# Performance work log

Hardware: AMD Instinct MI355X
Metric: run time of the kernel (lower is better)

The kernel has to match this reference:

```python
import jax, jax.numpy as jnp
import numpy as np
import math

B, L, DM = 8, 4096, 512            # batch, seq len (LQ == LK required by mean-fill quirk), model dim
DK, DV, C = 512, 512, 5            # projected dims, sampling factor
U_K = min(int(C * math.ceil(math.log(L))), L)  # 45 sampled keys
U_Q = min(int(C * math.ceil(math.log(L))), L)  # 45 top queries
SCALE = 1.0 / math.sqrt(DM)        # original divides by sqrt(d) where d = input dm


def setup_inputs() -> dict:
    key = jax.random.key(0)
    ks = jax.random.split(key, 10)
    w = 1.0 / math.sqrt(DM)
    # sample key indices per batch WITHOUT replacement (matches jax.random.choice(replace=False))
    kidx = jax.vmap(lambda k: jax.random.choice(k, L, shape=(U_K,), replace=False))(
        jax.random.split(ks[9], B)).astype(jnp.int32)
    return {
        "Q": jax.random.normal(ks[0], (B, L, DM), jnp.float32),
        "K": jax.random.normal(ks[1], (B, L, DM), jnp.float32),
        "V": jax.random.normal(ks[2], (B, L, DM), jnp.float32),
        "WQ": jax.random.normal(ks[3], (DM, DK), jnp.float32) * w,
        "bQ": jnp.zeros((DK,), jnp.float32),
        "WK": jax.random.normal(ks[4], (DM, DK), jnp.float32) * w,
        "bK": jnp.zeros((DK,), jnp.float32),
        "WV": jax.random.normal(ks[5], (DM, DV), jnp.float32) * w,
        "bV": jnp.zeros((DV,), jnp.float32),
        "kidx": kidx,
    }


def reference(Q, K, V, WQ, bQ, WK, bK, WV, bV, kidx):
    # dense projections (compute-dominant)
    Qp = Q @ WQ + bQ          # [B, L, DK]
    Kp = K @ WK + bK          # [B, L, DK]
    Vp = V @ WV + bV          # [B, L, DV]

    def per_sample(qp, kp, vp, idx):
        kbar = kp[idx]                                 # [U_K, DK] random key gather
        sbar = qp @ kbar.T                             # [L, U_K] sampled scores
        meas = jnp.max(sbar, axis=1) - jnp.mean(sbar, axis=1)  # sparsity measurement [L]
        _, I = jax.lax.top_k(meas, U_Q)                # top-u query indices
        qbar = qp[I]                                   # [U_Q, DK]
        attn = jax.nn.softmax(qbar @ kp.T * SCALE, axis=-1)    # [U_Q, L]
        s1 = attn @ vp                                 # [U_Q, DV]
        # faithful quirk: mean over FEATURE axis of V, broadcast to [L, DV]
        base = jnp.broadcast_to(jnp.mean(vp, axis=1, keepdims=True), (L, DV))
        return base.at[I].set(s1)                      # scatter selected rows

    return jax.vmap(per_sample)(Qp, Kp, Vp, kidx)      # [B, L, DV]
```

## Files before the change

kernel.cpp:

```cpp
#include <hip/hip_runtime.h>
#include <math.h>

static constexpr int B_ = 8;
static constexpr int L_ = 4096;
static constexpr int D_ = 512;
static constexpr int U_ = 45;
static constexpr float SCALE_ = 0.04419417382415922f;

static constexpr size_t OFF_WVMEAN = 0;
static constexpr size_t OFF_BV     = 512;
static constexpr size_t OFF_WQT    = 576;
static constexpr size_t OFF_WKT    = OFF_WQT + 262144;
static constexpr size_t OFF_KBAR   = OFF_WKT + 262144;
static constexpr size_t OFF_KW     = OFF_KBAR + 184320;
static constexpr size_t OFF_CVEC   = OFF_KW + 184320;
static constexpr size_t OFF_MEAS   = OFF_CVEC + 384;
static constexpr size_t OFF_TOPI   = OFF_MEAS + 32768;
static constexpr size_t OFF_QBAR   = OFF_TOPI + 384;
static constexpr size_t OFF_QW     = OFF_QBAR + 184320;
static constexpr size_t OFF_DVEC   = OFF_QW + 184320;
static constexpr size_t OFF_SC     = OFF_DVEC + 384;
static constexpr size_t OFF_PART   = OFF_SC + 1474560;
static constexpr size_t OFF_SMMX   = OFF_PART + 1474560;
static constexpr size_t OFF_SMIV   = OFF_SMMX + 512;
static constexpr size_t OFF_S1     = OFF_SMIV + 512;

__device__ __forceinline__ float wave_sum(float v) {
  #pragma unroll
  for (int m = 32; m; m >>= 1) v += __shfl_xor(v, m, 64);
  return v;
}
__device__ __forceinline__ float wave_max(float v) {
  #pragma unroll
  for (int m = 32; m; m >>= 1) v = fmaxf(v, __shfl_xor(v, m, 64));
  return v;
}

__global__ __launch_bounds__(256) void prep_k(const float* __restrict__ WQ,
    const float* __restrict__ WK, float* __restrict__ wqt, float* __restrict__ wkt,
    const float* __restrict__ WV, const float* __restrict__ bV,
    float* __restrict__ wvmean, float* __restrict__ bvout) {
  const int z = blockIdx.z;
  const int t = threadIdx.x + threadIdx.y * 32;
  if (z < 2) {
    const float* src = z ? WK : WQ;
    float* dst = z ? wkt : wqt;
    __shared__ float tile[32][33];
    int tx = threadIdx.x, ty = threadIdx.y;
    int x = blockIdx.x * 32 + tx;
    int y0 = blockIdx.y * 32;
    for (int r = ty; r < 32; r += 8) tile[r][tx] = src[(size_t)(y0 + r) * 512 + x];
    __syncthreads();
    int xo = y0 + tx;
    int yo0 = blockIdx.x * 32;
    for (int r = ty; r < 32; r += 8) dst[(size_t)(yo0 + r) * 512 + xo] = tile[tx][r];
    return;
  }
  if (blockIdx.y != 0 || blockIdx.x >= 8) return;
  int w = t >> 6, lane = t & 63;
  const float4* W4 = (const float4*)WV;
  int mbase = (blockIdx.x * 4 + w) * 16;
  for (int i = 0; i < 16; ++i) {
    int m = mbase + i;
    float4 a = W4[(size_t)m * 128 + lane];
    float4 c = W4[(size_t)m * 128 + 64 + lane];
    float s = ((a.x + a.y) + (a.z + a.w)) + ((c.x + c.y) + (c.z + c.w));
    s = wave_sum(s);
    if (lane == 0) wvmean[m] = s * (1.0f / 512.0f);
  }
  if (blockIdx.x == 0 && w == 0) {
    const float4* b4 = (const float4*)bV;
    float4 a = b4[lane], c = b4[64 + lane];
    float s = ((a.x + a.y) + (a.z + a.w)) + ((c.x + c.y) + (c.z + c.w));
    s = wave_sum(s);
    if (lane == 0) bvout[0] = s * (1.0f / 512.0f);
  }
}

__global__ __launch_bounds__(512) void projpair_k(const float* __restrict__ src,
    const int* __restrict__ idx, const float* __restrict__ W1, const float* __restrict__ b1,
    const float* __restrict__ avec, float* __restrict__ aux,
    const float* __restrict__ W2T, float* __restrict__ outp) {
  const int blk = blockIdx.x;
  const int b = blk / U_, j = blk % U_;
  const int t = threadIdx.x;
  __shared__ float rowA[512];
  __shared__ float rowB[512];
  __shared__ float red[8];

  const float* srow = idx ? (src + ((size_t)b * L_ + idx[b * U_ + j]) * 512)
                          : (src + ((size_t)(b * U_ + j)) * 512);
  rowA[t] = srow[t];
  __syncthreads();

  float a = b1[t];
  #pragma unroll 8
  for (int m = 0; m < 512; ++m) a = fmaf(rowA[m], W1[(size_t)m * 512 + t], a);

  if (aux) {
    float v = wave_sum(a * avec[t]);
    if ((t & 63) == 0) red[t >> 6] = v;
  }
  rowB[t] = a;
  __syncthreads();
  if (aux && t == 0) {
    float s2 = 0.f;
    #pragma unroll
    for (int k = 0; k < 8; ++k) s2 += red[k];
    aux[b * U_ + j] = s2;
  }

  float o = 0.f;
  #pragma unroll 8
  for (int m = 0; m < 512; ++m) o = fmaf(rowB[m], W2T[(size_t)m * 512 + t], o);
  outp[((size_t)(b * U_ + j)) * 512 + t] = o;
}

__global__ __launch_bounds__(512) void s1red_k(const float* __restrict__ part,
    const float* __restrict__ WV, const float* __restrict__ bV, float* __restrict__ s1) {
  const int blk = blockIdx.x;
  const int t = threadIdx.x;
  __shared__ float rowA[512];
  const size_t base = (size_t)blk * 512 + t;
  float s = 0.f;
  #pragma unroll
  for (int ls = 0; ls < 8; ++ls) s += part[(size_t)ls * 184320 + base];
  rowA[t] = s;
  __syncthreads();
  float o = bV[t];
  #pragma unroll 8
  for (int m = 0; m < 512; ++m) o = fmaf(rowA[m], WV[(size_t)m * 512 + t], o);
  s1[(size_t)blk * 512 + t] = o;
}

__global__ __launch_bounds__(256) void meas2_k(const float* __restrict__ Q,
    const float* __restrict__ kw, const float* __restrict__ cvec, float* __restrict__ meas) {
  const int b = blockIdx.y;
  const int l0 = blockIdx.x * 64;
  const int t = threadIdx.x;
  const int tx = t & 15, ty = t >> 4;
  const int rswz = (ty >> 1) & 3;

  __shared__ float Qs[64][68];
  __shared__ float Ks[48][68];

  float acc[4][3];
  #pragma unroll
  for (int i = 0; i < 4; ++i) { acc[i][0] = 0.f; acc[i][1] = 0.f; acc[i][2] = 0.f; }

  const float4* Q4  = (const float4*)(Q + ((size_t)b * L_ + l0) * 512);
  const float4* kw4 = (const float4*)(kw + (size_t)b * U_ * 512);

  float4 pq[4], pk[3];
  int lr[4], lc[4], kr[3], kc[3];
  #pragma unroll
  for (int p = 0; p < 4; ++p) { int idx = p * 256 + t; lr[p] = idx >> 4; lc[p] = idx & 15; }
  #pragma unroll
  for (int p = 0; p < 3; ++p) { int idx = p * 256 + t; kr[p] = idx >> 4; kc[p] = idx & 15; }

  #pragma unroll
  for (int p = 0; p < 4; ++p) pq[p] = Q4[(size_t)lr[p] * 128 + lc[p]];
  #pragma unroll
  for (int p = 0; p < 3; ++p)
    pk[p] = (kr[p] < U_) ? kw4[(size_t)kr[p] * 128 + kc[p]] : make_float4(0.f, 0.f, 0.f, 0.f);

  #pragma unroll
  for (int p = 0; p < 4; ++p) {
    int sw = (lr[p] >> 3) & 3;
    *(float4*)&Qs[lr[p]][(lc[p] ^ sw) * 4] = pq[p];
  }
  #pragma unroll
  for (int p = 0; p < 3; ++p) *(float4*)&Ks[kr[p]][kc[p] * 4] = pk[p];
  __syncthreads();

  for (int it = 0; it < 8; ++it) {
    if (it < 7) {
      int k0 = (it + 1) * 16;
      #pragma unroll
      for (int p = 0; p < 4; ++p) pq[p] = Q4[(size_t)lr[p] * 128 + k0 + lc[p]];
      #pragma unroll
      for (int p = 0; p < 3; ++p)
        pk[p] = (kr[p] < U_) ? kw4[(size_t)kr[p] * 128 + k0 + kc[p]] : make_float4(0.f, 0.f, 0.f, 0.f);
    }
    #pragma unroll 4
    for (int kk4 = 0; kk4 < 16; ++kk4) {
      float4 kv0 = *(const float4*)&Ks[tx * 3 + 0][kk4 * 4];
      float4 kv1 = *(const float4*)&Ks[tx * 3 + 1][kk4 * 4];
      float4 kv2 = *(const float4*)&Ks[tx * 3 + 2][kk4 * 4];
      int qc = (kk4 ^ rswz) * 4;
      #pragma unroll
      for (int i = 0; i < 4; ++i) {
        float4 qv = *(const float4*)&Qs[ty * 4 + i][qc];
        acc[i][0] = fmaf(qv.x, kv0.x, acc[i][0]); acc[i][0] = fmaf(qv.y, kv0.y, acc[i][0]);
        acc[i][0] = fmaf(qv.z, kv0.z, acc[i][0]); acc[i][0] = fmaf(qv.w, kv0.w, acc[i][0]);
        acc[i][1] = fmaf(qv.x, kv1.x, acc[i][1]); acc[i][1] = fmaf(qv.y, kv1.y, acc[i][1]);
        acc[i][1] = fmaf(qv.z, kv1.z, acc[i][1]); acc[i][1] = fmaf(qv.w, kv1.w, acc[i][1]);
        acc[i][2] = fmaf(qv.x, kv2.x, acc[i][2]); acc[i][2] = fmaf(qv.y, kv2.y, acc[i][2]);
        acc[i][2] = fmaf(qv.z, kv2.z, acc[i][2]); acc[i][2] = fmaf(qv.w, kv2.w, acc[i][2]);
      }
    }
    __syncthreads();
    if (it < 7) {
      #pragma unroll
      for (int p = 0; p < 4; ++p) {
        int sw = (lr[p] >> 3) & 3;
        *(float4*)&Qs[lr[p]][(lc[p] ^ sw) * 4] = pq[p];
      }
      #pragma unroll
      for (int p = 0; p < 3; ++p) *(float4*)&Ks[kr[p]][kc[p] * 4] = pk[p];
      __syncthreads();
    }
  }

  const bool valid = (tx < 15);
  float c0 = 0.f, c1 = 0.f, c2 = 0.f;
  if (valid) {
    c0 = cvec[b * U_ + tx * 3 + 0];
    c1 = cvec[b * U_ + tx * 3 + 1];
    c2 = cvec[b * U_ + tx * 3 + 2];
  }
  #pragma unroll
  for (int i = 0; i < 4; ++i) {
    float s0 = acc[i][0] + c0, s1 = acc[i][1] + c1, s2 = acc[i][2] + c2;
    float jmax = valid ? fmaxf(fmaxf(s0, s1), s2) : -3.4e38f;
    float jsum = valid ? (s0 + s1 + s2) : 0.f;
    #pragma unroll
    for (int m = 8; m; m >>= 1) {
      jmax = fmaxf(jmax, __shfl_xor(jmax, m, 64));
      jsum += __shfl_xor(jsum, m, 64);
    }
    if (tx == 0) meas[(size_t)b * L_ + l0 + ty * 4 + i] = jmax - jsum * (1.0f / 45.0f);
  }
}

__global__ __launch_bounds__(256) void scores2_k(const float* __restrict__ K,
    const float* __restrict__ qw, const float* __restrict__ dvec, float* __restrict__ sc) {
  const int b = blockIdx.y;
  const int l0 = blockIdx.x * 64;
  const int t = threadIdx.x;
  const int tx = t & 15, ty = t >> 4;
  const int rswz = (ty >> 1) & 3;

  __shared__ float Qs[64][68];
  __shared__ float Ks[48][68];

  float acc[4][3];
  #pragma unroll
  for (int i = 0; i < 4; ++i) { acc[i][0] = 0.f; acc[i][1] = 0.f; acc[i][2] = 0.f; }

  const float4* K4  = (const float4*)(K + ((size_t)b * L_ + l0) * 512);
  const float4* qw4 = (const float4*)(qw + (size_t)b * U_ * 512);

  float4 pq[4], pk[3];
  int lr[4], lc[4], kr[3], kc[3];
  #pragma unroll
  for (int p = 0; p < 4; ++p) { int idx = p * 256 + t; lr[p] = idx >> 4; lc[p] = idx & 15; }
  #pragma unroll
  for (int p = 0; p < 3; ++p) { int idx = p * 256 + t; kr[p] = idx >> 4; kc[p] = idx & 15; }

  #pragma unroll
  for (int p = 0; p < 4; ++p) pq[p] = K4[(size_t)lr[p] * 128 + lc[p]];
  #pragma unroll
  for (int p = 0; p < 3; ++p)
    pk[p] = (kr[p] < U_) ? qw4[(size_t)kr[p] * 128 + kc[p]] : make_float4(0.f, 0.f, 0.f, 0.f);

  #pragma unroll
  for (int p = 0; p < 4; ++p) {
    int sw = (lr[p] >> 3) & 3;
    *(float4*)&Qs[lr[p]][(lc[p] ^ sw) * 4] = pq[p];
  }
  #pragma unroll
  for (int p = 0; p < 3; ++p) *(float4*)&Ks[kr[p]][kc[p] * 4] = pk[p];
  __syncthreads();

  for (int it = 0; it < 8; ++it) {
    if (it < 7) {
      int k0 = (it + 1) * 16;
      #pragma unroll
      for (int p = 0; p < 4; ++p) pq[p] = K4[(size_t)lr[p] * 128 + k0 + lc[p]];
      #pragma unroll
      for (int p = 0; p < 3; ++p)
        pk[p] = (kr[p] < U_) ? qw4[(size_t)kr[p] * 128 + k0 + kc[p]] : make_float4(0.f, 0.f, 0.f, 0.f);
    }
    #pragma unroll 4
    for (int kk4 = 0; kk4 < 16; ++kk4) {
      float4 kv0 = *(const float4*)&Ks[tx * 3 + 0][kk4 * 4];
      float4 kv1 = *(const float4*)&Ks[tx * 3 + 1][kk4 * 4];
      float4 kv2 = *(const float4*)&Ks[tx * 3 + 2][kk4 * 4];
      int qc = (kk4 ^ rswz) * 4;
      #pragma unroll
      for (int i = 0; i < 4; ++i) {
        float4 qv = *(const float4*)&Qs[ty * 4 + i][qc];
        acc[i][0] = fmaf(qv.x, kv0.x, acc[i][0]); acc[i][0] = fmaf(qv.y, kv0.y, acc[i][0]);
        acc[i][0] = fmaf(qv.z, kv0.z, acc[i][0]); acc[i][0] = fmaf(qv.w, kv0.w, acc[i][0]);
        acc[i][1] = fmaf(qv.x, kv1.x, acc[i][1]); acc[i][1] = fmaf(qv.y, kv1.y, acc[i][1]);
        acc[i][1] = fmaf(qv.z, kv1.z, acc[i][1]); acc[i][1] = fmaf(qv.w, kv1.w, acc[i][1]);
        acc[i][2] = fmaf(qv.x, kv2.x, acc[i][2]); acc[i][2] = fmaf(qv.y, kv2.y, acc[i][2]);
        acc[i][2] = fmaf(qv.z, kv2.z, acc[i][2]); acc[i][2] = fmaf(qv.w, kv2.w, acc[i][2]);
      }
    }
    __syncthreads();
    if (it < 7) {
      #pragma unroll
      for (int p = 0; p < 4; ++p) {
        int sw = (lr[p] >> 3) & 3;
        *(float4*)&Qs[lr[p]][(lc[p] ^ sw) * 4] = pq[p];
      }
      #pragma unroll
      for (int p = 0; p < 3; ++p) *(float4*)&Ks[kr[p]][kc[p] * 4] = pk[p];
      __syncthreads();
    }
  }

  if (tx < 15) {
    float d0 = dvec[b * U_ + tx * 3 + 0];
    float d1 = dvec[b * U_ + tx * 3 + 1];
    float d2 = dvec[b * U_ + tx * 3 + 2];
    #pragma unroll
    for (int i = 0; i < 4; ++i) {
      int l = l0 + ty * 4 + i;
      sc[((size_t)(b * U_ + tx * 3 + 0)) * 4096 + l] = (acc[i][0] + d0) * SCALE_;
      sc[((size_t)(b * U_ + tx * 3 + 1)) * 4096 + l] = (acc[i][1] + d1) * SCALE_;
      sc[((size_t)(b * U_ + tx * 3 + 2)) * 4096 + l] = (acc[i][2] + d2) * SCALE_;
    }
  }
}

__global__ __launch_bounds__(256) void topk_k(const float* __restrict__ meas, int* __restrict__ topI) {
  int b = blockIdx.x, t = threadIdx.x;
  __shared__ unsigned long long keys[4096];
  __shared__ unsigned long long wred[4];
  for (int i = t; i < 4096; i += 256) {
    float m = meas[(size_t)b * 4096 + i];
    unsigned u = __float_as_uint(m);
    u = (u & 0x80000000u) ? ~u : (u | 0x80000000u);
    keys[i] = ((unsigned long long)u << 32) | (unsigned)(4095 - i);
  }
  __syncthreads();
  for (int it = 0; it < U_; ++it) {
    unsigned long long lm = 0ull;
    for (int i = t; i < 4096; i += 256) { unsigned long long k = keys[i]; lm = k > lm ? k : lm; }
    #pragma unroll
    for (int m = 32; m; m >>= 1) { unsigned long long o = __shfl_xor(lm, m, 64); lm = o > lm ? o : lm; }
    if ((t & 63) == 0) wred[t >> 6] = lm;
    __syncthreads();
    if (t == 0) {
      unsigned long long f = wred[0];
      for (int k2 = 1; k2 < 4; ++k2) f = wred[k2] > f ? wred[k2] : f;
      int idxl = 4095 - (int)(f & 0xFFFFFFFFull);
      topI[b * U_ + it] = idxl;
      keys[idxl] = 0ull;
    }
    __syncthreads();
  }
}

__global__ __launch_bounds__(256) void smred_k(const float* __restrict__ sc,
    float* __restrict__ mxb, float* __restrict__ ivb) {
  int row = blockIdx.x;
  int t = threadIdx.x;
  const float4* s4 = (const float4*)(sc + (size_t)row * 4096);
  __shared__ float red[4];
  float4 v[4];
  #pragma unroll
  for (int p = 0; p < 4; ++p) v[p] = s4[t + p * 256];
  float lmax = -3.4e38f;
  #pragma unroll
  for (int p = 0; p < 4; ++p)
    lmax = fmaxf(lmax, fmaxf(fmaxf(v[p].x, v[p].y), fmaxf(v[p].z, v[p].w)));
  lmax = wave_max(lmax);
  if ((t & 63) == 0) red[t >> 6] = lmax;
  __syncthreads();
  float mx = fmaxf(fmaxf(red[0], red[1]), fmaxf(red[2], red[3]));
  __syncthreads();
  float lsum = 0.f;
  #pragma unroll
  for (int p = 0; p < 4; ++p)
    lsum += expf(v[p].x - mx) + expf(v[p].y - mx) + expf(v[p].z - mx) + expf(v[p].w - mx);
  lsum = wave_sum(lsum);
  if ((t & 63) == 0) red[t >> 6] = lsum;
  __syncthreads();
  if (t == 0) {
    mxb[row] = mx;
    ivb[row] = 1.0f / (red[0] + red[1] + red[2] + red[3]);
  }
}

__device__ __forceinline__ float4 sm4(float4 v, float m, float iv) {
  return make_float4(expf(v.x - m) * iv, expf(v.y - m) * iv,
                     expf(v.z - m) * iv, expf(v.w - m) * iv);
}

__global__ __launch_bounds__(256) void attnv5_k(const float* __restrict__ V,
    const float* __restrict__ attn, const float* __restrict__ mxb,
    const float* __restrict__ ivb, float* __restrict__ part) {
  const int b = blockIdx.x, ks = blockIdx.y, dh = blockIdx.z;
  const int d0 = dh * 64;
  const int t = threadIdx.x;
  const int tx = t & 15, ty = t >> 4;

  __shared__ float As[2][48][68];
  __shared__ float Vs[2][64][68];

  const float* attnb = attn + (size_t)b * U_ * 4096 + (size_t)ks * 512;
  const float* Vb = V + ((size_t)b * L_ + (size_t)ks * 512) * 512 + d0;

  const int vrow = t >> 4, vc4 = t & 15;
  int arow[3], ac4[3], arr[3];
  float mxv[3], ivv[3];
  #pragma unroll
  for (int p = 0; p < 3; ++p) {
    int idx = p * 256 + t;
    arow[p] = idx >> 4; ac4[p] = idx & 15;
    arr[p] = arow[p] < U_ ? arow[p] : U_ - 1;
    mxv[p] = mxb[b * U_ + arr[p]];
    ivv[p] = ivb[b * U_ + arr[p]];
  }

  float4 pv0, pv1, pv2, pv3, pa0, pa1, pa2;

#define ISSUE(S) do { const int lb_ = (S) * 64;                                  \
    pv0 = *(const float4*)&Vb[(size_t)(lb_ + vrow +  0) * 512 + vc4 * 4];        \
    pv1 = *(const float4*)&Vb[(size_t)(lb_ + vrow + 16) * 512 + vc4 * 4];        \
    pv2 = *(const float4*)&Vb[(size_t)(lb_ + vrow + 32) * 512 + vc4 * 4];        \
    pv3 = *(const float4*)&Vb[(size_t)(lb_ + vrow + 48) * 512 + vc4 * 4];        \
    pa0 = *(const float4*)&attnb[(size_t)arr[0] * 4096 + lb_ + ac4[0] * 4];      \
    pa1 = *(const float4*)&attnb[(size_t)arr[1] * 4096 + lb_ + ac4[1] * 4];      \
    pa2 = *(const float4*)&attnb[(size_t)arr[2] * 4096 + lb_ + ac4[2] * 4];      \
  } while (0)

#define COMMIT(BUF) do {                                                         \
    *(float4*)&Vs[BUF][vrow +  0][vc4 * 4] = pv0;                                \
    *(float4*)&Vs[BUF][vrow + 16][vc4 * 4] = pv1;                                \
    *(float4*)&Vs[BUF][vrow + 32][vc4 * 4] = pv2;                                \
    *(float4*)&Vs[BUF][vrow + 48][vc4 * 4] = pv3;                                \
    *(float4*)&As[BUF][arow[0]][ac4[0] * 4] = sm4(pa0, mxv[0], ivv[0]);          \
    *(float4*)&As[BUF][arow[1]][ac4[1] * 4] = sm4(pa1, mxv[1], ivv[1]);          \
    *(float4*)&As[BUF][arow[2]][ac4[2] * 4] = sm4(pa2, mxv[2], ivv[2]);          \
  } while (0)

  float4 acc0 = make_float4(0.f, 0.f, 0.f, 0.f);
  float4 acc1 = make_float4(0.f, 0.f, 0.f, 0.f);
  float4 acc2 = make_float4(0.f, 0.f, 0.f, 0.f);

  ISSUE(0);
  asm volatile("s_waitcnt vmcnt(0)" ::: "memory");
  COMMIT(0);
  ISSUE(1);
  asm volatile("s_waitcnt lgkmcnt(0)" ::: "memory");
  __builtin_amdgcn_s_barrier();
  __builtin_amdgcn_sched_barrier(0);

  #pragma unroll 1
  for (int s = 0; s < 8; ++s) {
    const int rb = s & 1;
    #pragma unroll 4
    for (int l4 = 0; l4 < 16; ++l4) {
      float4 q0 = *(const float4*)&As[rb][tx * 3 + 0][l4 * 4];
      float4 q1 = *(const float4*)&As[rb][tx * 3 + 1][l4 * 4];
      float4 q2 = *(const float4*)&As[rb][tx * 3 + 2][l4 * 4];
      #pragma unroll
      for (int j = 0; j < 4; ++j) {
        float4 v = *(const float4*)&Vs[rb][l4 * 4 + j][ty * 4];
        float a0 = (j == 0) ? q0.x : (j == 1) ? q0.y : (j == 2) ? q0.z : q0.w;
        float a1 = (j == 0) ? q1.x : (j == 1) ? q1.y : (j == 2) ? q1.z : q1.w;
        float a2 = (j == 0) ? q2.x : (j == 1) ? q2.y : (j == 2) ? q2.z : q2.w;
        acc0.x = fmaf(a0, v.x, acc0.x); acc0.y = fmaf(a0, v.y, acc0.y);
        acc0.z = fmaf(a0, v.z, acc0.z); acc0.w = fmaf(a0, v.w, acc0.w);
        acc1.x = fmaf(a1, v.x, acc1.x); acc1.y = fmaf(a1, v.y, acc1.y);
        acc1.z = fmaf(a1, v.z, acc1.z); acc1.w = fmaf(a1, v.w, acc1.w);
        acc2.x = fmaf(a2, v.x, acc2.x); acc2.y = fmaf(a2, v.y, acc2.y);
        acc2.z = fmaf(a2, v.z, acc2.z); acc2.w = fmaf(a2, v.w, acc2.w);
      }
    }
    if (s + 1 < 8) {
      asm volatile("s_waitcnt vmcnt(0)" ::: "memory");
      COMMIT((s + 1) & 1);
      if (s + 2 < 8) ISSUE(s + 2);
      asm volatile("s_waitcnt lgkmcnt(0)" ::: "memory");
      __builtin_amdgcn_s_barrier();
      __builtin_amdgcn_sched_barrier(0);
    }
  }
#undef ISSUE
#undef COMMIT

  {
    float* dstbase = part + (((size_t)(ks * 8 + b)) * U_) * 512 + d0 + ty * 4;
    int i0 = tx * 3;
    if (i0 + 0 < U_) *(float4*)(dstbase + (size_t)(i0 + 0) * 512) = acc0;
    if (i0 + 1 < U_) *(float4*)(dstbase + (size_t)(i0 + 1) * 512) = acc1;
    if (i0 + 2 < U_) *(float4*)(dstbase + (size_t)(i0 + 2) * 512) = acc2;
  }
}

__global__ __launch_bounds__(256) void output_k(const float* __restrict__ V,
    const float* __restrict__ wvmean, const float* __restrict__ bvp,
    const int* __restrict__ topI, const float* __restrict__ s1, float* __restrict__ outp) {
  int b = blockIdx.y, tile = blockIdx.x;
  int l0 = tile * 64;
  int t = threadIdx.x, w = t >> 6, lane = t & 63;
  __shared__ int sel[64];
  if (t < 64) sel[t] = -1;
  __syncthreads();
  if (t < U_) {
    int lj = topI[b * U_ + t] - l0;
    if (lj >= 0 && lj < 64) sel[lj] = t;
  }
  __syncthreads();
  const float4* wv4 = (const float4*)wvmean;
  float4 wa = wv4[lane], wb = wv4[64 + lane];
  float bv = bvp[0];
  const float4* V4 = (const float4*)(V + (size_t)b * L_ * 512);
  float4* out4 = (float4*)(outp + (size_t)b * L_ * 512);
  const float4* s14 = (const float4*)s1;
  for (int r = w; r < 64; r += 4) {
    int l = l0 + r;
    int j = sel[r];
    float4 o1, o2;
    if (j >= 0) {
      o1 = s14[((size_t)(b * U_ + j)) * 128 + lane];
      o2 = s14[((size_t)(b * U_ + j)) * 128 + 64 + lane];
    } else {
      float4 va = V4[(size_t)l * 128 + lane];
      float4 vb = V4[(size_t)l * 128 + 64 + lane];
      float s = va.x * wa.x + va.y * wa.y + va.z * wa.z + va.w * wa.w
              + vb.x * wb.x + vb.y * wb.y + vb.z * wb.z + vb.w * wb.w;
      s = wave_sum(s);
      float base = s + bv;
      o1 = make_float4(base, base, base, base);
      o2 = o1;
    }
    out4[(size_t)l * 128 + lane] = o1;
    out4[(size_t)l * 128 + 64 + lane] = o2;
  }
}

extern "C" void kernel_launch(void* const* d_in, const int* in_sizes, int n_in,
                              void* d_out, int out_size, void* d_ws, size_t ws_size,
                              hipStream_t stream) {
  (void)in_sizes; (void)n_in; (void)out_size; (void)ws_size;
  const float* Q  = (const float*)d_in[0];
  const float* K  = (const float*)d_in[1];
  const float* V  = (const float*)d_in[2];
  const float* WQ = (const float*)d_in[3];
  const float* bQ = (const float*)d_in[4];
  const float* WK = (const float*)d_in[5];
  const float* bK = (const float*)d_in[6];
  const float* WV = (const float*)d_in[7];
  const float* bV = (const float*)d_in[8];
  const int* kidx = (const int*)d_in[9];
  float* ws = (float*)d_ws;
  float* out = (float*)d_out;

  float* wvmean = ws + OFF_WVMEAN;
  float* bvm    = ws + OFF_BV;
  float* wqt    = ws + OFF_WQT;
  float* wkt    = ws + OFF_WKT;
  float* kw     = ws + OFF_KW;
  float* cvec   = ws + OFF_CVEC;
  float* measp  = ws + OFF_MEAS;
  int*   topI   = (int*)(ws + OFF_TOPI);
  float* qw     = ws + OFF_QW;
  float* dvec   = ws + OFF_DVEC;
  float* sc     = ws + OFF_SC;
  float* partp  = ws + OFF_PART;
  float* mxb    = ws + OFF_SMMX;
  float* ivb    = ws + OFF_SMIV;
  float* s1     = ws + OFF_S1;

  prep_k<<<dim3(16, 16, 3), dim3(32, 8), 0, stream>>>(WQ, WK, wqt, wkt, WV, bV, wvmean, bvm);

  projpair_k<<<dim3(360), dim3(512), 0, stream>>>(K, kidx, WK, bK, bQ, cvec, wqt, kw);
  meas2_k<<<dim3(64, 8), dim3(256), 0, stream>>>(Q, kw, cvec, measp);
  topk_k<<<dim3(8), dim3(256), 0, stream>>>(measp, topI);
  projpair_k<<<dim3(360), dim3(512), 0, stream>>>(Q, topI, WQ, bQ, bK, dvec, wkt, qw);
  scores2_k<<<dim3(64, 8), dim3(256), 0, stream>>>(K, qw, dvec, sc);
  smred_k<<<dim3(360), dim3(256), 0, stream>>>(sc, mxb, ivb);
  attnv5_k<<<dim3(8, 8, 8), dim3(256), 0, stream>>>(V, sc, mxb, ivb, partp);
  s1red_k<<<dim3(360), dim3(512), 0, stream>>>(partp, WV, bV, s1);
  output_k<<<dim3(64, 8), dim3(256), 0, stream>>>(V, wvmean, bvm, topI, s1, out);
}
```

Baseline: 364.0 us.

## Double-buffer LDS tiles in meas and scores kernels with explicit waitcnt pipeline

Replaces the single-buffered shared-memory tiles in the two skinny GEMM kernels (meas and scores) with double-buffered tiles behind a shared macro pipeline. This cuts the two barriers per k-step to one, and uses explicit s_waitcnt and s_barrier instructions so global loads for step s+2 overlap compute on step s. Padding rows of the weight tile now load a clamped valid row instead of taking a zero branch. Shared memory per block doubles, which could lower occupancy, and the hand-placed waitcnt and sched_barrier ordering carries correctness and scheduling risk.

```diff
diff --git a/kernel.cpp b/kernel.cpp
--- a/kernel.cpp
+++ b/kernel.cpp
@@ -133,84 +133,85 @@
   s1[(size_t)blk * 512 + t] = o;
 }
 
-__global__ __launch_bounds__(256) void meas2_k(const float* __restrict__ Q,
+
+#define M2P_DECLS                                                              \
+  const int t = threadIdx.x;                                                   \
+  const int tx = t & 15, ty = t >> 4;                                          \
+  const int rswz = (ty >> 1) & 3;                                              \
+  __shared__ float Qs[2][64][68];                                              \
+  __shared__ float Ks[2][48][68];                                              \
+  int lr[4], lc[4], kr[3], kc[3], krr[3];                                      \
+  _Pragma("unroll") for (int p = 0; p < 4; ++p) {                              \
+    int idx = p * 256 + t; lr[p] = idx >> 4; lc[p] = idx & 15; }               \
+  _Pragma("unroll") for (int p = 0; p < 3; ++p) {                              \
+    int idx = p * 256 + t; kr[p] = idx >> 4; kc[p] = idx & 15;                 \
+    krr[p] = kr[p] < U_ ? kr[p] : U_ - 1; }                                    \
+  float4 pq[4], pk[3];                                                         \
+  float acc[4][3];                                                             \
+  _Pragma("unroll") for (int i = 0; i < 4; ++i) {                              \
+    acc[i][0] = 0.f; acc[i][1] = 0.f; acc[i][2] = 0.f; }
+
+#define M2P_ISSUE(S) do { const int k0_ = (S) * 16;                            \
+    _Pragma("unroll") for (int p = 0; p < 4; ++p)                              \
+      pq[p] = X4[(size_t)lr[p] * 128 + k0_ + lc[p]];                           \
+    _Pragma("unroll") for (int p = 0; p < 3; ++p)                              \
+      pk[p] = W4[(size_t)krr[p] * 128 + k0_ + kc[p]];                          \
+  } while (0)
+
+#define M2P_COMMIT(B) do {                                                     \
+    _Pragma("unroll") for (int p = 0; p < 4; ++p) {                            \
+      int sw = (lr[p] >> 3) & 3;                                               \
+      *(float4*)&Qs[B][lr[p]][(lc[p] ^ sw) * 4] = pq[p];                       \
+    }                                                                          \
+    _Pragma("unroll") for (int p = 0; p < 3; ++p)                              \
+      *(float4*)&Ks[B][kr[p]][kc[p] * 4] = pk[p];                              \
+  } while (0)
+
+#define M2P_PIPELINE                                                           \
+  M2P_ISSUE(0);                                                                \
+  asm volatile("s_waitcnt vmcnt(0)" ::: "memory");                             \
+  M2P_COMMIT(0);                                                               \
+  M2P_ISSUE(1);                                                                \
+  asm volatile("s_waitcnt lgkmcnt(0)" ::: "memory");                           \
+  __builtin_amdgcn_s_barrier();                                                \
+  __builtin_amdgcn_sched_barrier(0);                                           \
+  _Pragma("unroll 1")                                                          \
+  for (int s = 0; s < 8; ++s) {                                                \
+    const int rb = s & 1;                                                      \
+    _Pragma("unroll 4")                                                        \
+    for (int kk4 = 0; kk4 < 16; ++kk4) {                                       \
+      float4 kv0 = *(const float4*)&Ks[rb][tx * 3 + 0][kk4 * 4];               \
+      float4 kv1 = *(const float4*)&Ks[rb][tx * 3 + 1][kk4 * 4];               \
+      float4 kv2 = *(const float4*)&Ks[rb][tx * 3 + 2][kk4 * 4];               \
+      int qc = (kk4 ^ rswz) * 4;                                               \
+      _Pragma("unroll") for (int i = 0; i < 4; ++i) {                          \
+        float4 qv = *(const float4*)&Qs[rb][ty * 4 + i][qc];                   \
+        acc[i][0] = fmaf(qv.x, kv0.x, acc[i][0]); acc[i][0] = fmaf(qv.y, kv0.y, acc[i][0]); \
+        acc[i][0] = fmaf(qv.z, kv0.z, acc[i][0]); acc[i][0] = fmaf(qv.w, kv0.w, acc[i][0]); \
+        acc[i][1] = fmaf(qv.x, kv1.x, acc[i][1]); acc[i][1] = fmaf(qv.y, kv1.y, acc[i][1]); \
+        acc[i][1] = fmaf(qv.z, kv1.z, acc[i][1]); acc[i][1] = fmaf(qv.w, kv1.w, acc[i][1]); \
+        acc[i][2] = fmaf(qv.x, kv2.x, acc[i][2]); acc[i][2] = fmaf(qv.y, kv2.y, acc[i][2]); \
+        acc[i][2] = fmaf(qv.z, kv2.z, acc[i][2]); acc[i][2] = fmaf(qv.w, kv2.w, acc[i][2]); \
+      }                                                                        \
+    }                                                                          \
+    if (s + 1 < 8) {                                                           \
+      asm volatile("s_waitcnt vmcnt(0)" ::: "memory");                         \
+      M2P_COMMIT((s + 1) & 1);                                                 \
+      if (s + 2 < 8) M2P_ISSUE(s + 2);                                         \
+      asm volatile("s_waitcnt lgkmcnt(0)" ::: "memory");                       \
+      __builtin_amdgcn_s_barrier();                                            \
+      __builtin_amdgcn_sched_barrier(0);                                       \
+    }                                                                          \
+  }
+
+__global__ __launch_bounds__(256) void meas2p_k(const float* __restrict__ Q,
     const float* __restrict__ kw, const float* __restrict__ cvec, float* __restrict__ meas) {
   const int b = blockIdx.y;
   const int l0 = blockIdx.x * 64;
-  const int t = threadIdx.x;
-  const int tx = t & 15, ty = t >> 4;
-  const int rswz = (ty >> 1) & 3;
-
-  __shared__ float Qs[64][68];
-  __shared__ float Ks[48][68];
-
-  float acc[4][3];
-  #pragma unroll
-  for (int i = 0; i < 4; ++i) { acc[i][0] = 0.f; acc[i][1] = 0.f; acc[i][2] = 0.f; }
-
-  const float4* Q4  = (const float4*)(Q + ((size_t)b * L_ + l0) * 512);
-  const float4* kw4 = (const float4*)(kw + (size_t)b * U_ * 512);
-
-  float4 pq[4], pk[3];
-  int lr[4], lc[4], kr[3], kc[3];
-  #pragma unroll
-  for (int p = 0; p < 4; ++p) { int idx = p * 256 + t; lr[p] = idx >> 4; lc[p] = idx & 15; }
-  #pragma unroll
-  for (int p = 0; p < 3; ++p) { int idx = p * 256 + t; kr[p] = idx >> 4; kc[p] = idx & 15; }
-
-  #pragma unroll
-  for (int p = 0; p < 4; ++p) pq[p] = Q4[(size_t)lr[p] * 128 + lc[p]];
-  #pragma unroll
-  for (int p = 0; p < 3; ++p)
-    pk[p] = (kr[p] < U_) ? kw4[(size_t)kr[p] * 128 + kc[p]] : make_float4(0.f, 0.f, 0.f, 0.f);
-
-  #pragma unroll
-  for (int p = 0; p < 4; ++p) {
-    int sw = (lr[p] >> 3) & 3;
-    *(float4*)&Qs[lr[p]][(lc[p] ^ sw) * 4] = pq[p];
-  }
-  #pragma unroll
-  for (int p = 0; p < 3; ++p) *(float4*)&Ks[kr[p]][kc[p] * 4] = pk[p];
-  __syncthreads();
-
-  for (int it = 0; it < 8; ++it) {
-    if (it < 7) {
-      int k0 = (it + 1) * 16;
-      #pragma unroll
-      for (int p = 0; p < 4; ++p) pq[p] = Q4[(size_t)lr[p] * 128 + k0 + lc[p]];
-      #pragma unroll
-      for (int p = 0; p < 3; ++p)
-        pk[p] = (kr[p] < U_) ? kw4[(size_t)kr[p] * 128 + k0 + kc[p]] : make_float4(0.f, 0.f, 0.f, 0.f);
-    }
-    #pragma unroll 4
-    for (int kk4 = 0; kk4 < 16; ++kk4) {
-      float4 kv0 = *(const float4*)&Ks[tx * 3 + 0][kk4 * 4];
-      float4 kv1 = *(const float4*)&Ks[tx * 3 + 1][kk4 * 4];
-      float4 kv2 = *(const float4*)&Ks[tx * 3 + 2][kk4 * 4];
-      int qc = (kk4 ^ rswz) * 4;
-      #pragma unroll
-      for (int i = 0; i < 4; ++i) {
-        float4 qv = *(const float4*)&Qs[ty * 4 + i][qc];
-        acc[i][0] = fmaf(qv.x, kv0.x, acc[i][0]); acc[i][0] = fmaf(qv.y, kv0.y, acc[i][0]);
-        acc[i][0] = fmaf(qv.z, kv0.z, acc[i][0]); acc[i][0] = fmaf(qv.w, kv0.w, acc[i][0]);
-        acc[i][1] = fmaf(qv.x, kv1.x, acc[i][1]); acc[i][1] = fmaf(qv.y, kv1.y, acc[i][1]);
-        acc[i][1] = fmaf(qv.z, kv1.z, acc[i][1]); acc[i][1] = fmaf(qv.w, kv1.w, acc[i][1]);
-        acc[i][2] = fmaf(qv.x, kv2.x, acc[i][2]); acc[i][2] = fmaf(qv.y, kv2.y, acc[i][2]);
-        acc[i][2] = fmaf(qv.z, kv2.z, acc[i][2]); acc[i][2] = fmaf(qv.w, kv2.w, acc[i][2]);
-      }
-    }
-    __syncthreads();
-    if (it < 7) {
-      #pragma unroll
-      for (int p = 0; p < 4; ++p) {
-        int sw = (lr[p] >> 3) & 3;
-        *(float4*)&Qs[lr[p]][(lc[p] ^ sw) * 4] = pq[p];
-      }
-      #pragma unroll
-      for (int p = 0; p < 3; ++p) *(float4*)&Ks[kr[p]][kc[p] * 4] = pk[p];
-      __syncthreads();
-    }
-  }
+  const float4* X4 = (const float4*)(Q + ((size_t)b * L_ + l0) * 512);
+  const float4* W4 = (const float4*)(kw + (size_t)b * U_ * 512);
+  M2P_DECLS
+  M2P_PIPELINE
 
   const bool valid = (tx < 15);
   float c0 = 0.f, c1 = 0.f, c2 = 0.f;
@@ -233,84 +234,14 @@
   }
 }
 
-__global__ __launch_bounds__(256) void scores2_k(const float* __restrict__ K,
+__global__ __launch_bounds__(256) void scores2p_k(const float* __restrict__ K,
     const float* __restrict__ qw, const float* __restrict__ dvec, float* __restrict__ sc) {
   const int b = blockIdx.y;
   const int l0 = blockIdx.x * 64;
-  const int t = threadIdx.x;
-  const int tx = t & 15, ty = t >> 4;
-  const int rswz = (ty >> 1) & 3;
-
-  __shared__ float Qs[64][68];
-  __shared__ float Ks[48][68];
-
-  float acc[4][3];
-  #pragma unroll
-  for (int i = 0; i < 4; ++i) { acc[i][0] = 0.f; acc[i][1] = 0.f; acc[i][2] = 0.f; }
-
-  const float4* K4  = (const float4*)(K + ((size_t)b * L_ + l0) * 512);
-  const float4* qw4 = (const float4*)(qw + (size_t)b * U_ * 512);
-
-  float4 pq[4], pk[3];
-  int lr[4], lc[4], kr[3], kc[3];
-  #pragma unroll
-  for (int p = 0; p < 4; ++p) { int idx = p * 256 + t; lr[p] = idx >> 4; lc[p] = idx & 15; }
-  #pragma unroll
-  for (int p = 0; p < 3; ++p) { int idx = p * 256 + t; kr[p] = idx >> 4; kc[p] = idx & 15; }
-
-  #pragma unroll
-  for (int p = 0; p < 4; ++p) pq[p] = K4[(size_t)lr[p] * 128 + lc[p]];
-  #pragma unroll
-  for (int p = 0; p < 3; ++p)
-    pk[p] = (kr[p] < U_) ? qw4[(size_t)kr[p] * 128 + kc[p]] : make_float4(0.f, 0.f, 0.f, 0.f);
-
-  #pragma unroll
-  for (int p = 0; p < 4; ++p) {
-    int sw = (lr[p] >> 3) & 3;
-    *(float4*)&Qs[lr[p]][(lc[p] ^ sw) * 4] = pq[p];
-  }
-  #pragma unroll
-  for (int p = 0; p < 3; ++p) *(float4*)&Ks[kr[p]][kc[p] * 4] = pk[p];
-  __syncthreads();
-
-  for (int it = 0; it < 8; ++it) {
-    if (it < 7) {
-      int k0 = (it + 1) * 16;
-      #pragma unroll
-      for (int p = 0; p < 4; ++p) pq[p] = K4[(size_t)lr[p] * 128 + k0 + lc[p]];
-      #pragma unroll
-      for (int p = 0; p < 3; ++p)
-        pk[p] = (kr[p] < U_) ? qw4[(size_t)kr[p] * 128 + k0 + kc[p]] : make_float4(0.f, 0.f, 0.f, 0.f);
-    }
-    #pragma unroll 4
-    for (int kk4 = 0; kk4 < 16; ++kk4) {
-      float4 kv0 = *(const float4*)&Ks[tx * 3 + 0][kk4 * 4];
-      float4 kv1 = *(const float4*)&Ks[tx * 3 + 1][kk4 * 4];
-      float4 kv2 = *(const float4*)&Ks[tx * 3 + 2][kk4 * 4];
-      int qc = (kk4 ^ rswz) * 4;
-      #pragma unroll
-      for (int i = 0; i < 4; ++i) {
-        float4 qv = *(const float4*)&Qs[ty * 4 + i][qc];
-        acc[i][0] = fmaf(qv.x, kv0.x, acc[i][0]); acc[i][0] = fmaf(qv.y, kv0.y, acc[i][0]);
-        acc[i][0] = fmaf(qv.z, kv0.z, acc[i][0]); acc[i][0] = fmaf(qv.w, kv0.w, acc[i][0]);
-        acc[i][1] = fmaf(qv.x, kv1.x, acc[i][1]); acc[i][1] = fmaf(qv.y, kv1.y, acc[i][1]);
-        acc[i][1] = fmaf(qv.z, kv1.z, acc[i][1]); acc[i][1] = fmaf(qv.w, kv1.w, acc[i][1]);
-        acc[i][2] = fmaf(qv.x, kv2.x, acc[i][2]); acc[i][2] = fmaf(qv.y, kv2.y, acc[i][2]);
-        acc[i][2] = fmaf(qv.z, kv2.z, acc[i][2]); acc[i][2] = fmaf(qv.w, kv2.w, acc[i][2]);
-      }
-    }
-    __syncthreads();
-    if (it < 7) {
-      #pragma unroll
-      for (int p = 0; p < 4; ++p) {
-        int sw = (lr[p] >> 3) & 3;
-        *(float4*)&Qs[lr[p]][(lc[p] ^ sw) * 4] = pq[p];
-      }
-      #pragma unroll
-      for (int p = 0; p < 3; ++p) *(float4*)&Ks[kr[p]][kc[p] * 4] = pk[p];
-      __syncthreads();
-    }
-  }
+  const float4* X4 = (const float4*)(K + ((size_t)b * L_ + l0) * 512);
+  const float4* W4 = (const float4*)(qw + (size_t)b * U_ * 512);
+  M2P_DECLS
+  M2P_PIPELINE
 
   if (tx < 15) {
     float d0 = dvec[b * U_ + tx * 3 + 0];
@@ -325,6 +256,11 @@
     }
   }
 }
+
+#undef M2P_DECLS
+#undef M2P_ISSUE
+#undef M2P_COMMIT
+#undef M2P_PIPELINE
 
 __global__ __launch_bounds__(256) void topk_k(const float* __restrict__ meas, int* __restrict__ topI) {
   int b = blockIdx.x, t = threadIdx.x;
@@ -572,10 +508,10 @@
   prep_k<<<dim3(16, 16, 3), dim3(32, 8), 0, stream>>>(WQ, WK, wqt, wkt, WV, bV, wvmean, bvm);
 
   projpair_k<<<dim3(360), dim3(512), 0, stream>>>(K, kidx, WK, bK, bQ, cvec, wqt, kw);
-  meas2_k<<<dim3(64, 8), dim3(256), 0, stream>>>(Q, kw, cvec, measp);
+  meas2p_k<<<dim3(64, 8), dim3(256), 0, stream>>>(Q, kw, cvec, measp);
   topk_k<<<dim3(8), dim3(256), 0, stream>>>(measp, topI);
   projpair_k<<<dim3(360), dim3(512), 0, stream>>>(Q, topI, WQ, bQ, bK, dvec, wkt, qw);
-  scores2_k<<<dim3(64, 8), dim3(256), 0, stream>>>(K, qw, dvec, sc);
+  scores2p_k<<<dim3(64, 8), dim3(256), 0, stream>>>(K, qw, dvec, sc);
   smred_k<<<dim3(360), dim3(256), 0, stream>>>(sc, mxb, ivb);
   attnv5_k<<<dim3(8, 8, 8), dim3(256), 0, stream>>>(V, sc, mxb, ivb, partp);
   s1red_k<<<dim3(360), dim3(512), 0, stream>>>(partp, WV, bV, s1);
```

After: 395.9 us. +8.8%, slower.

## Split reduction dimension of sampled-score GEMMs across two blocks with combine kernels

Applied to the files above, without the earlier changes.

The meas and scores kernels become one split-K kernel that handles half of the 512-wide reduction per block (grid z=2) and writes partial sums to scratch buffers. New combine kernels add the two halves and apply the bias and max-minus-mean, or the bias and scale. This doubles the block count (512 to 1024) to fill more CUs on a dense GEMM with few output columns. In exchange it adds two kernel launches and extra global traffic for the partial-sum round trip.

```diff
diff --git a/kernel.cpp b/kernel.cpp
--- a/kernel.cpp
+++ b/kernel.cpp
@@ -133,10 +133,11 @@
   s1[(size_t)blk * 512 + t] = o;
 }
 
-__global__ __launch_bounds__(256) void meas2_k(const float* __restrict__ Q,
-    const float* __restrict__ kw, const float* __restrict__ cvec, float* __restrict__ meas) {
+__global__ __launch_bounds__(256) void dotsplit_k(const float* __restrict__ X,
+    const float* __restrict__ W, float* __restrict__ p0, float* __restrict__ p1) {
   const int b = blockIdx.y;
   const int l0 = blockIdx.x * 64;
+  const int z = blockIdx.z;
   const int t = threadIdx.x;
   const int tx = t & 15, ty = t >> 4;
   const int rswz = (ty >> 1) & 3;
@@ -148,21 +149,24 @@
   #pragma unroll
   for (int i = 0; i < 4; ++i) { acc[i][0] = 0.f; acc[i][1] = 0.f; acc[i][2] = 0.f; }
 
-  const float4* Q4  = (const float4*)(Q + ((size_t)b * L_ + l0) * 512);
-  const float4* kw4 = (const float4*)(kw + (size_t)b * U_ * 512);
+  const float4* X4 = (const float4*)(X + ((size_t)b * L_ + l0) * 512);
+  const float4* W4 = (const float4*)(W + (size_t)b * U_ * 512);
+  const int kb = z * 64;
 
   float4 pq[4], pk[3];
-  int lr[4], lc[4], kr[3], kc[3];
+  int lr[4], lc[4], kr[3], kc[3], krr[3];
   #pragma unroll
   for (int p = 0; p < 4; ++p) { int idx = p * 256 + t; lr[p] = idx >> 4; lc[p] = idx & 15; }
   #pragma unroll
-  for (int p = 0; p < 3; ++p) { int idx = p * 256 + t; kr[p] = idx >> 4; kc[p] = idx & 15; }
-
-  #pragma unroll
-  for (int p = 0; p < 4; ++p) pq[p] = Q4[(size_t)lr[p] * 128 + lc[p]];
-  #pragma unroll
-  for (int p = 0; p < 3; ++p)
-    pk[p] = (kr[p] < U_) ? kw4[(size_t)kr[p] * 128 + kc[p]] : make_float4(0.f, 0.f, 0.f, 0.f);
+  for (int p = 0; p < 3; ++p) {
+    int idx = p * 256 + t; kr[p] = idx >> 4; kc[p] = idx & 15;
+    krr[p] = kr[p] < U_ ? kr[p] : U_ - 1;
+  }
+
+  #pragma unroll
+  for (int p = 0; p < 4; ++p) pq[p] = X4[(size_t)lr[p] * 128 + kb + lc[p]];
+  #pragma unroll
+  for (int p = 0; p < 3; ++p) pk[p] = W4[(size_t)krr[p] * 128 + kb + kc[p]];
 
   #pragma unroll
   for (int p = 0; p < 4; ++p) {
@@ -173,14 +177,13 @@
   for (int p = 0; p < 3; ++p) *(float4*)&Ks[kr[p]][kc[p] * 4] = pk[p];
   __syncthreads();
 
-  for (int it = 0; it < 8; ++it) {
-    if (it < 7) {
-      int k0 = (it + 1) * 16;
+  for (int it = 0; it < 4; ++it) {
+    if (it < 3) {
+      int k0 = kb + (it + 1) * 16;
       #pragma unroll
-      for (int p = 0; p < 4; ++p) pq[p] = Q4[(size_t)lr[p] * 128 + k0 + lc[p]];
+      for (int p = 0; p < 4; ++p) pq[p] = X4[(size_t)lr[p] * 128 + k0 + lc[p]];
       #pragma unroll
-      for (int p = 0; p < 3; ++p)
-        pk[p] = (kr[p] < U_) ? kw4[(size_t)kr[p] * 128 + k0 + kc[p]] : make_float4(0.f, 0.f, 0.f, 0.f);
+      for (int p = 0; p < 3; ++p) pk[p] = W4[(size_t)krr[p] * 128 + k0 + kc[p]];
     }
     #pragma unroll 4
     for (int kk4 = 0; kk4 < 16; ++kk4) {
@@ -200,7 +203,7 @@
       }
     }
     __syncthreads();
-    if (it < 7) {
+    if (it < 3) {
       #pragma unroll
       for (int p = 0; p < 4; ++p) {
         int sw = (lr[p] >> 3) & 3;
@@ -212,118 +215,55 @@
     }
   }
 
-  const bool valid = (tx < 15);
-  float c0 = 0.f, c1 = 0.f, c2 = 0.f;
-  if (valid) {
-    c0 = cvec[b * U_ + tx * 3 + 0];
-    c1 = cvec[b * U_ + tx * 3 + 1];
-    c2 = cvec[b * U_ + tx * 3 + 2];
-  }
-  #pragma unroll
-  for (int i = 0; i < 4; ++i) {
-    float s0 = acc[i][0] + c0, s1 = acc[i][1] + c1, s2 = acc[i][2] + c2;
-    float jmax = valid ? fmaxf(fmaxf(s0, s1), s2) : -3.4e38f;
-    float jsum = valid ? (s0 + s1 + s2) : 0.f;
-    #pragma unroll
-    for (int m = 8; m; m >>= 1) {
-      jmax = fmaxf(jmax, __shfl_xor(jmax, m, 64));
-      jsum += __shfl_xor(jsum, m, 64);
-    }
-    if (tx == 0) meas[(size_t)b * L_ + l0 + ty * 4 + i] = jmax - jsum * (1.0f / 45.0f);
-  }
-}
-
-__global__ __launch_bounds__(256) void scores2_k(const float* __restrict__ K,
-    const float* __restrict__ qw, const float* __restrict__ dvec, float* __restrict__ sc) {
-  const int b = blockIdx.y;
-  const int l0 = blockIdx.x * 64;
+  float* dst = z ? p1 : p0;
+  #pragma unroll
+  for (int r = 0; r < 3; ++r) {
+    int j = tx * 3 + r;
+    if (j < U_) {
+      *(float4*)&dst[((size_t)(b * U_ + j)) * 4096 + l0 + ty * 4] =
+          make_float4(acc[0][r], acc[1][r], acc[2][r], acc[3][r]);
+    }
+  }
+}
+
+__global__ __launch_bounds__(256) void meascomb_k(const float* __restrict__ p0,
+    const float* __restrict__ p1, const float* __restrict__ cvec, float* __restrict__ meas) {
+  const int b = blockIdx.y, l0 = blockIdx.x * 64;
   const int t = threadIdx.x;
-  const int tx = t & 15, ty = t >> 4;
-  const int rswz = (ty >> 1) & 3;
-
-  __shared__ float Qs[64][68];
-  __shared__ float Ks[48][68];
-
-  float acc[4][3];
-  #pragma unroll
-  for (int i = 0; i < 4; ++i) { acc[i][0] = 0.f; acc[i][1] = 0.f; acc[i][2] = 0.f; }
-
-  const float4* K4  = (const float4*)(K + ((size_t)b * L_ + l0) * 512);
-  const float4* qw4 = (const float4*)(qw + (size_t)b * U_ * 512);
-
-  float4 pq[4], pk[3];
-  int lr[4], lc[4], kr[3], kc[3];
-  #pragma unroll
-  for (int p = 0; p < 4; ++p) { int idx = p * 256 + t; lr[p] = idx >> 4; lc[p] = idx & 15; }
-  #pragma unroll
-  for (int p = 0; p < 3; ++p) { int idx = p * 256 + t; kr[p] = idx >> 4; kc[p] = idx & 15; }
-
-  #pragma unroll
-  for (int p = 0; p < 4; ++p) pq[p] = K4[(size_t)lr[p] * 128 + lc[p]];
-  #pragma unroll
-  for (int p = 0; p < 3; ++p)
-    pk[p] = (kr[p] < U_) ? qw4[(size_t)kr[p] * 128 + kc[p]] : make_float4(0.f, 0.f, 0.f, 0.f);
-
-  #pragma unroll
-  for (int p = 0; p < 4; ++p) {
-    int sw = (lr[p] >> 3) & 3;
-    *(float4*)&Qs[lr[p]][(lc[p] ^ sw) * 4] = pq[p];
-  }
-  #pragma unroll
-  for (int p = 0; p < 3; ++p) *(float4*)&Ks[kr[p]][kc[p] * 4] = pk[p];
-  __syncthreads();
-
-  for (int it = 0; it < 8; ++it) {
-    if (it < 7) {
-      int k0 = (it + 1) * 16;
-      #pragma unroll
-      for (int p = 0; p < 4; ++p) pq[p] = K4[(size_t)lr[p] * 128 + k0 + lc[p]];
-      #pragma unroll
-      for (int p = 0; p < 3; ++p)
-        pk[p] = (kr[p] < U_) ? qw4[(size_t)kr[p] * 128 + k0 + kc[p]] : make_float4(0.f, 0.f, 0.f, 0.f);
-    }
-    #pragma unroll 4
-    for (int kk4 = 0; kk4 < 16; ++kk4) {
-      float4 kv0 = *(const float4*)&Ks[tx * 3 + 0][kk4 * 4];
-      float4 kv1 = *(const float4*)&Ks[tx * 3 + 1][kk4 * 4];
-      float4 kv2 = *(const float4*)&Ks[tx * 3 + 2][kk4 * 4];
-      int qc = (kk4 ^ rswz) * 4;
-      #pragma unroll
-      for (int i = 0; i < 4; ++i) {
-        float4 qv = *(const float4*)&Qs[ty * 4 + i][qc];
-        acc[i][0] = fmaf(qv.x, kv0.x, acc[i][0]); acc[i][0] = fmaf(qv.y, kv0.y, acc[i][0]);
-        acc[i][0] = fmaf(qv.z, kv0.z, acc[i][0]); acc[i][0] = fmaf(qv.w, kv0.w, acc[i][0]);
-        acc[i][1] = fmaf(qv.x, kv1.x, acc[i][1]); acc[i][1] = fmaf(qv.y, kv1.y, acc[i][1]);
-        acc[i][1] = fmaf(qv.z, kv1.z, acc[i][1]); acc[i][1] = fmaf(qv.w, kv1.w, acc[i][1]);
-        acc[i][2] = fmaf(qv.x, kv2.x, acc[i][2]); acc[i][2] = fmaf(qv.y, kv2.y, acc[i][2]);
-        acc[i][2] = fmaf(qv.z, kv2.z, acc[i][2]); acc[i][2] = fmaf(qv.w, kv2.w, acc[i][2]);
-      }
-    }
-    __syncthreads();
-    if (it < 7) {
-      #pragma unroll
-      for (int p = 0; p < 4; ++p) {
-        int sw = (lr[p] >> 3) & 3;
-        *(float4*)&Qs[lr[p]][(lc[p] ^ sw) * 4] = pq[p];
-      }
-      #pragma unroll
-      for (int p = 0; p < 3; ++p) *(float4*)&Ks[kr[p]][kc[p] * 4] = pk[p];
-      __syncthreads();
-    }
-  }
-
-  if (tx < 15) {
-    float d0 = dvec[b * U_ + tx * 3 + 0];
-    float d1 = dvec[b * U_ + tx * 3 + 1];
-    float d2 = dvec[b * U_ + tx * 3 + 2];
-    #pragma unroll
-    for (int i = 0; i < 4; ++i) {
-      int l = l0 + ty * 4 + i;
-      sc[((size_t)(b * U_ + tx * 3 + 0)) * 4096 + l] = (acc[i][0] + d0) * SCALE_;
-      sc[((size_t)(b * U_ + tx * 3 + 1)) * 4096 + l] = (acc[i][1] + d1) * SCALE_;
-      sc[((size_t)(b * U_ + tx * 3 + 2)) * 4096 + l] = (acc[i][2] + d2) * SCALE_;
-    }
-  }
+  __shared__ float buf[45][68];
+  for (int idx = t; idx < 45 * 16; idx += 256) {
+    int j = idx >> 4, c4 = idx & 15;
+    size_t off = ((size_t)(b * U_ + j)) * 4096 + l0 + c4 * 4;
+    float4 a = *(const float4*)&p0[off];
+    float4 c = *(const float4*)&p1[off];
+    *(float4*)&buf[j][c4 * 4] = make_float4(a.x + c.x, a.y + c.y, a.z + c.z, a.w + c.w);
+  }
+  __syncthreads();
+  int l = t >> 2, q = t & 3;
+  float mx = -3.4e38f, sm = 0.f;
+  for (int j = q; j < U_; j += 4) {
+    float s = buf[j][l] + cvec[b * U_ + j];
+    mx = fmaxf(mx, s);
+    sm += s;
+  }
+  #pragma unroll
+  for (int m = 1; m < 4; m <<= 1) {
+    mx = fmaxf(mx, __shfl_xor(mx, m, 64));
+    sm += __shfl_xor(sm, m, 64);
+  }
+  if (q == 0) meas[(size_t)b * L_ + l0 + l] = mx - sm * (1.0f / 45.0f);
+}
+
+__global__ __launch_bounds__(256) void scorescomb_k(const float* __restrict__ p0,
+    const float* __restrict__ dvec, float* __restrict__ sc) {
+  int x4 = blockIdx.x * 256 + threadIdx.x;
+  int bj = x4 >> 10;
+  float dj = dvec[bj];
+  const float4* a4 = (const float4*)p0;
+  float4* c4p = (float4*)sc;
+  float4 a = a4[x4], c = c4p[x4];
+  c4p[x4] = make_float4((a.x + c.x + dj) * SCALE_, (a.y + c.y + dj) * SCALE_,
+                        (a.z + c.z + dj) * SCALE_, (a.w + c.w + dj) * SCALE_);
 }
 
 __global__ __launch_bounds__(256) void topk_k(const float* __restrict__ meas, int* __restrict__ topI) {
@@ -572,10 +512,12 @@
   prep_k<<<dim3(16, 16, 3), dim3(32, 8), 0, stream>>>(WQ, WK, wqt, wkt, WV, bV, wvmean, bvm);
 
   projpair_k<<<dim3(360), dim3(512), 0, stream>>>(K, kidx, WK, bK, bQ, cvec, wqt, kw);
-  meas2_k<<<dim3(64, 8), dim3(256), 0, stream>>>(Q, kw, cvec, measp);
+  dotsplit_k<<<dim3(64, 8, 2), dim3(256), 0, stream>>>(Q, kw, partp, sc);
+  meascomb_k<<<dim3(64, 8), dim3(256), 0, stream>>>(partp, sc, cvec, measp);
   topk_k<<<dim3(8), dim3(256), 0, stream>>>(measp, topI);
   projpair_k<<<dim3(360), dim3(512), 0, stream>>>(Q, topI, WQ, bQ, bK, dvec, wkt, qw);
-  scores2_k<<<dim3(64, 8), dim3(256), 0, stream>>>(K, qw, dvec, sc);
+  dotsplit_k<<<dim3(64, 8, 2), dim3(256), 0, stream>>>(K, qw, partp, sc);
+  scorescomb_k<<<dim3(1440), dim3(256), 0, stream>>>(partp, dvec, sc);
   smred_k<<<dim3(360), dim3(256), 0, stream>>>(sc, mxb, ivb);
   attnv5_k<<<dim3(8, 8, 8), dim3(256), 0, stream>>>(V, sc, mxb, ivb, partp);
   s1red_k<<<dim3(360), dim3(512), 0, stream>>>(partp, WV, bV, s1);
```

Result: slower. 379.3 us (+4.2%).
